# Performance work log

Hardware: AMD Instinct MI355X
Metric: run time of the kernel (lower is better)

## Reference

```python
import jax, jax.numpy as jnp
import numpy as np

TP, TN = 0.03, 0.03   # top-k fractions (module init args)
TS, TC = 0.03, 0.07   # sigmoid sharpness, contrastive temperature
EPS_PD = 1e-6         # torch F.pairwise_distance eps


def _l2norm(x, axis):
    # F.normalize(p=2) with eps clamp 1e-12
    return x / jnp.maximum(jnp.linalg.norm(x, axis=axis, keepdims=True), 1e-12)


def setup_inputs() -> dict:
    key = jax.random.key(0)
    k = jax.random.split(key, 5)
    B, C, H, W = 192, 512, 28, 28
    return {
        "ev": jax.random.normal(k[0], (B, C, H, W), jnp.float32),
        "ea": jax.random.normal(k[1], (B, 2048), jnp.float32),
        "Wv": jax.random.normal(k[2], (C, C), jnp.float32) * 0.04,
        "Wa1": jax.random.normal(k[3], (512, 2048), jnp.float32) * 0.02,
        "Wa2": jax.random.normal(k[4], (512, 512), jnp.float32) * 0.04,
    }


def reference(ev, ea, Wv, Wa1, Wa2):
    B, C, H, W = ev.shape
    HW = H * W
    tp = int(HW * TP)
    tn = int(HW * TN)

    # audio projection (frozen encoder output ea -> fa)
    fa = jax.nn.relu(ea @ Wa1.T) @ Wa2.T            # [B, 512]

    # visual 1x1-conv projection + GAP
    fv_map = jnp.einsum('bchw,oc->bohw', ev, Wv)    # [B, C, H, W]
    ind_vec = fv_map.mean(axis=(2, 3))              # [B, C]

    fv_norm = _l2norm(fv_map, axis=1)               # per-pixel channel L2 norm
    iv_norm = _l2norm(ind_vec, axis=1)              # [B, C]

    # Sij[b,d,p] = <fv_norm[b,:,p], iv_norm[d,:]>
    S = jnp.einsum('bchw,dc->bdhw', fv_norm, iv_norm).reshape(B, B, HW)

    # data-dependent per-(b,d) top-k thresholds
    pos_thr = jax.lax.top_k(S, tp)[0][..., -1:]     # tp-th largest
    neg_thr = -jax.lax.top_k(-S, tn)[0][..., -1:]   # tn-th smallest

    m_p = jax.nn.sigmoid((S - pos_thr) / TS)
    m_n = 1.0 - jax.nn.sigmoid((S - neg_thr) / TS)

    SP = (S * m_p).sum(-1) / m_p.sum(-1)            # [B, B]
    SN = (S * m_n).sum(-1) / m_n.sum(-1)            # [B, B]

    logits1 = jnp.concatenate([SP, SN], axis=1) / TC      # [B, 2B]
    logits2 = jnp.concatenate([SP.T, SN.T], axis=1) / TC  # [B, 2B]
    labels = jnp.arange(B)

    def ce(logits):
        logp = jax.nn.log_softmax(logits, axis=-1)
        return -jnp.take_along_axis(logp, labels[:, None], axis=1).mean()

    loss1 = ce(logits1)
    loss2 = ce(logits2)

    eye = jnp.eye(B, dtype=S.dtype)
    mask = eye - (1.0 - eye) / (B - 1)

    # squared pairwise distance between detached ind_vec and fa (torch eps)
    iv_d = jax.lax.stop_gradient(ind_vec)
    diff = iv_d[:, None, :] - fa[None, :, :] + EPS_PD
    dist = (diff * diff).sum(-1)                    # [B, B]

    ivn_d = jax.lax.stop_gradient(iv_norm)
    vv = ivn_d @ ivn_d.T
    w = -vv * (1.0 - eye) + eye
    dist = dist * w

    loss3 = jnp.maximum((dist * mask).sum(1) + 0.6, 0.0).mean()
    loss4 = jnp.maximum((dist * mask).sum(0) + 0.6, 0.0).mean()

    return ((loss1 + loss2) / 2, (loss3 + loss4) / 2)
```

## Files before the change

### kernel.cpp

```cpp
#include <hip/hip_runtime.h>
#include <hip/hip_fp8.h>
#include <math.h>

#define B_   192
#define C_   512
#define HW_  784
#define TPK  23
#define NTOT (B_ * HW_)
#define SCL  0x7F7F7F7F

typedef __attribute__((ext_vector_type(4))) float f4;
typedef __attribute__((ext_vector_type(16))) float f16v;
typedef __attribute__((ext_vector_type(8))) int i8i;
typedef __attribute__((ext_vector_type(4))) unsigned int u4i;
typedef __attribute__((ext_vector_type(8))) unsigned char uc8;

__device__ __forceinline__ float sigf(float x) {
    return 1.0f / (1.0f + __expf(-x));
}
__device__ __forceinline__ unsigned short f2bf(float f) {
    unsigned u = __float_as_uint(f);
    unsigned r = u + 0x7FFFu + ((u >> 16) & 1u);
    return (unsigned short)(r >> 16);
}
__device__ __forceinline__ float bf2f(unsigned short u) {
    return __uint_as_float(((unsigned)u) << 16);
}
__device__ __forceinline__ unsigned char f2fp8(float x) {
    __hip_fp8_e4m3 t(x);
    return (unsigned char)t.__x;
}
__device__ __forceinline__ void gld16(const void* g, void* l) {
    __builtin_amdgcn_global_load_lds((const __attribute__((address_space(1))) unsigned int*)g,
                                     (__attribute__((address_space(3))) unsigned int*)l, 16, 0, 0);
}
__device__ __forceinline__ i8i frag32(const unsigned char* base, int c0, int c1) {
    u4i lo = *(const u4i*)(base + c0);
    u4i hi = *(const u4i*)(base + c1);
    i8i r;
    r[0] = (int)lo[0]; r[1] = (int)lo[1]; r[2] = (int)lo[2]; r[3] = (int)lo[3];
    r[4] = (int)hi[0]; r[5] = (int)hi[1]; r[6] = (int)hi[2]; r[7] = (int)hi[3];
    return r;
}

__global__ void k_evmean(const float* __restrict__ ev, float* __restrict__ evmean) {
    int row  = blockIdx.x * 4 + (threadIdx.x >> 6);
    int lane = threadIdx.x & 63;
    const float4* s4 = (const float4*)(ev + (size_t)row * HW_);
    float s = 0.f;
    for (int i = lane; i < HW_ / 4; i += 64) {
        float4 v = s4[i];
        s += v.x + v.y + v.z + v.w;
    }
    for (int off = 32; off > 0; off >>= 1) s += __shfl_down(s, off, 64);
    if (lane == 0) evmean[row] = s * (1.0f / HW_);
}

template<int BKN, int RELUA, int SPLITK>
__global__ __launch_bounds__(256)
void k32(const float* __restrict__ A, const float* __restrict__ B,
         float* __restrict__ C, int M, int N, int K) {
    __shared__ float As[16][68];
    __shared__ float Bs[16][68];
    int m0 = blockIdx.y * 64, n0 = blockIdx.x * 64;
    int kslice = K / SPLITK;
    int kbeg = blockIdx.z * kslice;
    int tid = threadIdx.x;
    int tx = tid & 15, ty = tid >> 4;
    int r = tid >> 2, c4 = tid & 3;

    float acc[4][4];
#pragma unroll
    for (int i = 0; i < 4; i++)
#pragma unroll
        for (int j = 0; j < 4; j++) acc[i][j] = 0.f;

    for (int k0 = kbeg; k0 < kbeg + kslice; k0 += 16) {
        float4 av = *(const float4*)(A + (size_t)(m0 + r) * K + k0 + c4 * 4);
        if (RELUA) {
            av.x = fmaxf(av.x, 0.f); av.y = fmaxf(av.y, 0.f);
            av.z = fmaxf(av.z, 0.f); av.w = fmaxf(av.w, 0.f);
        }
        As[c4 * 4 + 0][r] = av.x; As[c4 * 4 + 1][r] = av.y;
        As[c4 * 4 + 2][r] = av.z; As[c4 * 4 + 3][r] = av.w;
        if (BKN == 0) {
            float4 bv = *(const float4*)(B + (size_t)(n0 + r) * K + k0 + c4 * 4);
            Bs[c4 * 4 + 0][r] = bv.x; Bs[c4 * 4 + 1][r] = bv.y;
            Bs[c4 * 4 + 2][r] = bv.z; Bs[c4 * 4 + 3][r] = bv.w;
        } else {
            float4 bv = *(const float4*)(B + (size_t)(k0 + ty) * N + n0 + tx * 4);
            Bs[ty][tx * 4 + 0] = bv.x; Bs[ty][tx * 4 + 1] = bv.y;
            Bs[ty][tx * 4 + 2] = bv.z; Bs[ty][tx * 4 + 3] = bv.w;
        }
        __syncthreads();
#pragma unroll
        for (int kk = 0; kk < 16; kk++) {
            float a_[4];
#pragma unroll
            for (int i = 0; i < 4; i++) a_[i] = As[kk][ty * 4 + i];
            float4 bb = *(const float4*)&Bs[kk][tx * 4];
#pragma unroll
            for (int i = 0; i < 4; i++) {
                acc[i][0] = fmaf(a_[i], bb.x, acc[i][0]);
                acc[i][1] = fmaf(a_[i], bb.y, acc[i][1]);
                acc[i][2] = fmaf(a_[i], bb.z, acc[i][2]);
                acc[i][3] = fmaf(a_[i], bb.w, acc[i][3]);
            }
        }
        __syncthreads();
    }
#pragma unroll
    for (int i = 0; i < 4; i++) {
        if (SPLITK > 1) {
            float* row = C + (size_t)(m0 + ty * 4 + i) * N + n0 + tx * 4;
#pragma unroll
            for (int j = 0; j < 4; j++) atomicAdd(&row[j], acc[i][j]);
        } else {
            *(float4*)(C + (size_t)(m0 + ty * 4 + i) * N + n0 + tx * 4) =
                make_float4(acc[i][0], acc[i][1], acc[i][2], acc[i][3]);
        }
    }
}

__global__ void k_rownorm(const float* __restrict__ iv, float* __restrict__ ivn) {
    int b = blockIdx.x, lane = threadIdx.x;
    float v[8]; float s = 0.f;
#pragma unroll
    for (int k = 0; k < 8; k++) {
        v[k] = iv[(size_t)b * C_ + lane + 64 * k];
        s = fmaf(v[k], v[k], s);
    }
#pragma unroll
    for (int off = 32; off > 0; off >>= 1) s += __shfl_xor(s, off, 64);
    float rn = 1.0f / fmaxf(sqrtf(s), 1e-12f);
#pragma unroll
    for (int k = 0; k < 8; k++) ivn[(size_t)b * C_ + lane + 64 * k] = v[k] * rn;
}

__global__ void k_prepA(const float* __restrict__ Wv, unsigned char* __restrict__ Abf) {
    int r = blockIdx.x, tid = threadIdx.x;
    int row = (r < 512) ? r : (192 + r);
    int swz = ((row >> 1) & 3) << 4;
    for (int i = 0; i < 2; i++) {
        int c = tid + i * 256;
        float v = (r < 512) ? Wv[(size_t)r * C_ + c] : 0.f;
        Abf[(size_t)row * C_ + (c ^ swz)] = f2fp8(v);
    }
}

__global__ __launch_bounds__(256)
void k_Ufp8(const float* __restrict__ ivn, const float* __restrict__ Wv,
            unsigned char* __restrict__ Abf) {
    __shared__ float As[16][68];
    __shared__ float Bs[16][68];
    int m0 = blockIdx.y * 64, n0 = blockIdx.x * 64;
    int tid = threadIdx.x;
    int tx = tid & 15, ty = tid >> 4;
    int r = tid >> 2, c4 = tid & 3;
    float acc[4][4];
#pragma unroll
    for (int i = 0; i < 4; i++)
#pragma unroll
        for (int j = 0; j < 4; j++) acc[i][j] = 0.f;
    for (int k0 = 0; k0 < C_; k0 += 16) {
        float4 av = *(const float4*)(ivn + (size_t)(m0 + r) * C_ + k0 + c4 * 4);
        As[c4 * 4 + 0][r] = av.x; As[c4 * 4 + 1][r] = av.y;
        As[c4 * 4 + 2][r] = av.z; As[c4 * 4 + 3][r] = av.w;
        float4 bv = *(const float4*)(Wv + (size_t)(k0 + ty) * C_ + n0 + tx * 4);
        Bs[ty][tx * 4 + 0] = bv.x; Bs[ty][tx * 4 + 1] = bv.y;
        Bs[ty][tx * 4 + 2] = bv.z; Bs[ty][tx * 4 + 3] = bv.w;
        __syncthreads();
#pragma unroll
        for (int kk = 0; kk < 16; kk++) {
            float a_[4];
#pragma unroll
            for (int i = 0; i < 4; i++) a_[i] = As[kk][ty * 4 + i];
            float4 bb = *(const float4*)&Bs[kk][tx * 4];
#pragma unroll
            for (int i = 0; i < 4; i++) {
                acc[i][0] = fmaf(a_[i], bb.x, acc[i][0]);
                acc[i][1] = fmaf(a_[i], bb.y, acc[i][1]);
                acc[i][2] = fmaf(a_[i], bb.z, acc[i][2]);
                acc[i][3] = fmaf(a_[i], bb.w, acc[i][3]);
            }
        }
        __syncthreads();
    }
#pragma unroll
    for (int i = 0; i < 4; i++) {
        int orow = 512 + m0 + ty * 4 + i;
        int swz = ((orow >> 1) & 3) << 4;
        unsigned char* rowp = Abf + (size_t)orow * C_;
        int cphys = (n0 + tx * 4) ^ swz;
#pragma unroll
        for (int j = 0; j < 4; j++) rowp[cphys + j] = f2fp8(acc[i][j]);
    }
}

__global__ __launch_bounds__(256)
void k_transpose64(const float* __restrict__ ev, unsigned char* __restrict__ evT,
                   float* __restrict__ evsum, int doevm, int b0) {
    __shared__ float t[64][67];
    int bl = blockIdx.z, b = b0 + bl;
    int c0 = blockIdx.y * 64, p0 = blockIdx.x * 64;
    int tid = threadIdx.x;
    int cl = tid >> 4;
    int pc = tid & 15;
    int p = p0 + pc * 4;
#pragma unroll
    for (int q = 0; q < 4; q++) {
        int c_local = q * 16 + cl;
        const float* src = ev + ((size_t)b * C_ + c0 + c_local) * HW_;
        float4 v = make_float4(0.f, 0.f, 0.f, 0.f);
        if (p + 3 < HW_) v = *(const float4*)(src + p);
        else if (p < HW_) { for (int j = 0; j < 4; j++) if (p + j < HW_) ((float*)&v)[j] = src[p + j]; }
        if (doevm) {
            float rs = v.x + v.y + v.z + v.w;
            rs += __shfl_xor(rs, 1, 16);
            rs += __shfl_xor(rs, 2, 16);
            rs += __shfl_xor(rs, 4, 16);
            rs += __shfl_xor(rs, 8, 16);
            if (pc == 0) atomicAdd(&evsum[b * C_ + c0 + c_local], rs * (1.0f / HW_));
        }
        t[c_local][pc * 4 + 0] = v.x; t[c_local][pc * 4 + 1] = v.y;
        t[c_local][pc * 4 + 2] = v.z; t[c_local][pc * 4 + 3] = v.w;
    }
    __syncthreads();
    int r = tid >> 3;
    int j = tid & 7;
#pragma unroll
    for (int q = 0; q < 2; q++) {
        int prow = p0 + r + q * 32;
        if (prow < HW_) {
            size_t n = (size_t)bl * HW_ + prow;
            int swz = ((int)(n >> 1) & 3) << 4;
            uc8 o;
#pragma unroll
            for (int k = 0; k < 8; k++) o[k] = f2fp8(t[j * 8 + k][r + q * 32]);
            *(uc8*)(evT + n * C_ + c0 + ((j * 8) ^ swz)) = o;
        }
    }
}

__global__ __launch_bounds__(256, 4)
void k_gemm(const unsigned char* __restrict__ Abf, const unsigned char* __restrict__ evT,
            float* __restrict__ n2, unsigned short* __restrict__ Tb, int ntiles) {
    __shared__ unsigned char As[2][8192];
    __shared__ unsigned char Bs[2][8192];

    int id = blockIdx.x;
    int xcd = id & 7, slot = id >> 3;
    int S = (ntiles + 7) >> 3;
    int w = xcd * S + slot;
    if (w >= ntiles) return;
    int nt = w / 6, ot = w % 6;
    int o0 = ot * 128, n0 = nt * 128;

    int tid = threadIdx.x;
    int wid = tid >> 6, lane = tid & 63;
    int wy = wid >> 1, wx = wid & 1;
    int r31 = lane & 31, hi = lane >> 5;
    int swz = (r31 >> 1) & 3;
    int ch0 = ((2 * hi) ^ swz) * 16;
    int ch1 = ((2 * hi + 1) ^ swz) * 16;

    const unsigned char* Ag = Abf + ((size_t)o0 + (tid >> 2)) * C_ + (tid & 3) * 16;
    const unsigned char* Bg = evT + ((size_t)n0 + (tid >> 2)) * C_ + (tid & 3) * 16;
    int lds16 = tid * 16;

    f16v acc[2][2] = {};
    int cur = 0;

#define STAGE(buf, k0) do { \
    gld16(Ag + (k0),           &As[buf][0]    + lds16); \
    gld16(Ag + (k0) + 64 * C_, &As[buf][4096] + lds16); \
    gld16(Bg + (k0),           &Bs[buf][0]    + lds16); \
    gld16(Bg + (k0) + 64 * C_, &Bs[buf][4096] + lds16); \
} while (0)

    STAGE(0, 0);
    __syncthreads();
    for (int t = 0; t < 8; ++t) {
        if (t < 7) STAGE(cur ^ 1, (t + 1) * 64);
        const unsigned char* Ab = &As[cur][0];
        const unsigned char* Bb = &Bs[cur][0];
        i8i a[2], b[2];
#pragma unroll
        for (int mi = 0; mi < 2; mi++)
            a[mi] = frag32(Ab + (wy * 64 + mi * 32 + r31) * 64, ch0, ch1);
#pragma unroll
        for (int ni = 0; ni < 2; ni++)
            b[ni] = frag32(Bb + (wx * 64 + ni * 32 + r31) * 64, ch0, ch1);
#pragma unroll
        for (int mi = 0; mi < 2; mi++)
#pragma unroll
            for (int ni = 0; ni < 2; ni++)
                acc[mi][ni] = __builtin_amdgcn_mfma_scale_f32_32x32x64_f8f6f4(
                    a[mi], b[ni], acc[mi][ni], 0, 0, 0, SCL, 0, SCL);
        __syncthreads();
        cur ^= 1;
    }
#undef STAGE

    if (ot < 4) {
        float* red = (float*)&As[0][0];
#pragma unroll
        for (int ni = 0; ni < 2; ni++) {
            float s = 0.f;
#pragma unroll
            for (int mi = 0; mi < 2; mi++)
#pragma unroll
                for (int r = 0; r < 16; r++) { float x = acc[mi][ni][r]; s = fmaf(x, x, s); }
            red[(wy * 2 + hi) * 128 + wx * 64 + ni * 32 + r31] = s;
        }
        __syncthreads();
        if (tid < 128) {
            float s = 0.f;
#pragma unroll
            for (int q = 0; q < 4; q++) s += red[q * 128 + tid];
            atomicAdd(&n2[n0 + tid], s);
        }
    } else {
        int dbase = o0 - 512 + wy * 64;
        unsigned blv[2]; int pv[2];
#pragma unroll
        for (int ni = 0; ni < 2; ni++) {
            unsigned nn = (unsigned)(n0 + wx * 64 + ni * 32 + r31);
            blv[ni] = nn / 784u;
            pv[ni]  = (int)(nn - blv[ni] * 784u);
        }
#pragma unroll
        for (int mi = 0; mi < 2; mi++)
#pragma unroll
            for (int r = 0; r < 16; r++) {
                int dd = dbase + mi * 32 + (r & 3) + 8 * (r >> 2) + 4 * hi;
                if (dd < B_) {
#pragma unroll
                    for (int ni = 0; ni < 2; ni++)
                        Tb[((size_t)blv[ni] * B_ + dd) * HW_ + pv[ni]] = f2bf(acc[mi][ni][r]);
                }
            }
    }
}

__global__ void k_invn(const float* __restrict__ n2, float* __restrict__ invn, int n) {
    int i = blockIdx.x * 256 + threadIdx.x;
    if (i >= n) return;
    invn[i] = 1.0f / fmaxf(sqrtf(n2[i]), 1e-12f);
}

__global__ __launch_bounds__(256)
void k_pool(const unsigned short* __restrict__ T, const float* __restrict__ invn,
            float* __restrict__ SP, float* __restrict__ SN, int b0) {
    int tid = threadIdx.x;
    int wv = tid >> 6, lane = tid & 63;
    int d = blockIdx.x * 4 + wv;
    int bl = blockIdx.y, b = b0 + bl;
    const unsigned short* Trow = T + ((size_t)b * B_ + d) * HW_;
    const float* nrow = invn + (size_t)b * HW_;
    float sv[13];
#pragma unroll
    for (int i = 0; i < 12; i++) {
        int p = lane + i * 64;
        sv[i] = bf2f(Trow[p]) * nrow[p];
    }
    {
        int p = lane + 768;
        sv[12] = (p < HW_) ? bf2f(Trow[p]) * nrow[p] : __uint_as_float(0x7FC00000u);
    }
    float vmax = -1e30f, vmin = 1e30f;
#pragma unroll
    for (int i = 0; i < 13; i++) { vmax = fmaxf(vmax, sv[i]); vmin = fminf(vmin, sv[i]); }
#pragma unroll
    for (int off = 32; off > 0; off >>= 1) {
        vmax = fmaxf(vmax, __shfl_xor(vmax, off, 64));
        vmin = fminf(vmin, __shfl_xor(vmin, off, 64));
    }
    float lo1 = vmin, hi1 = vmax, lo2 = vmin, hi2 = vmax;
    for (int it = 0; it < 13; ++it) {
        float m1 = 0.5f * (lo1 + hi1), m2 = 0.5f * (lo2 + hi2);
        int c1 = 0, c2 = 0;
#pragma unroll
        for (int i = 0; i < 13; i++) {
            c1 += __popcll(__ballot(sv[i] >= m1));
            c2 += __popcll(__ballot(sv[i] <= m2));
        }
        if (c1 >= TPK) lo1 = m1; else hi1 = m1;
        if (c2 >= TPK) hi2 = m2; else lo2 = m2;
    }
    float thrp = lo1, thrn = hi2;
    const float its = 1.0f / 0.03f;
    float spn = 0.f, spd = 0.f, snn = 0.f, snd = 0.f;
#pragma unroll
    for (int i = 0; i < 13; i++) {
        if (i == 12 && lane >= 16) continue;
        float s = sv[i];
        float mp = sigf((s - thrp) * its);
        float mn = sigf(-(s - thrn) * its);
        spn += s * mp; spd += mp;
        snn += s * mn; snd += mn;
    }
    for (int off = 32; off > 0; off >>= 1) {
        spn += __shfl_down(spn, off, 64);
        spd += __shfl_down(spd, off, 64);
        snn += __shfl_down(snn, off, 64);
        snd += __shfl_down(snd, off, 64);
    }
    if (lane == 0) {
        SP[b * B_ + d] = spn / spd;
        SN[b * B_ + d] = snn / snd;
    }
}

__global__ void k_loss12(const float* __restrict__ SP, const float* __restrict__ SN,
                         float* __restrict__ acc) {
    __shared__ float red[128];
    int i = blockIdx.x, tid = threadIdx.x;
    const float itc = 1.0f / 0.07f;
    for (int phase = 0; phase < 2; phase++) {
        float mx = -INFINITY;
        for (int j = tid; j < 2 * B_; j += 128) {
            float v;
            if (phase == 0) v = (j < B_ ? SP[i * B_ + j] : SN[i * B_ + (j - B_)]);
            else            v = (j < B_ ? SP[j * B_ + i] : SN[(j - B_) * B_ + i]);
            mx = fmaxf(mx, v * itc);
        }
        red[tid] = mx; __syncthreads();
        for (int s = 64; s > 0; s >>= 1) { if (tid < s) red[tid] = fmaxf(red[tid], red[tid + s]); __syncthreads(); }
        mx = red[0]; __syncthreads();
        float se = 0.f;
        for (int j = tid; j < 2 * B_; j += 128) {
            float v;
            if (phase == 0) v = (j < B_ ? SP[i * B_ + j] : SN[i * B_ + (j - B_)]);
            else            v = (j < B_ ? SP[j * B_ + i] : SN[(j - B_) * B_ + i]);
            se += __expf(v * itc - mx);
        }
        red[tid] = se; __syncthreads();
        for (int s = 64; s > 0; s >>= 1) { if (tid < s) red[tid] += red[tid + s]; __syncthreads(); }
        if (tid == 0) {
            float lse = logf(red[0]) + mx;
            atomicAdd(&acc[phase], lse - SP[i * B_ + i] * itc);
        }
        __syncthreads();
    }
}

__global__ __launch_bounds__(256)
void k_distfin(const float* __restrict__ iv, const float* __restrict__ ivn,
               const float* __restrict__ fa, const float* __restrict__ acc,
               float* __restrict__ rowsum, float* __restrict__ colsum,
               int* __restrict__ cnt, float* __restrict__ out) {
    __shared__ float Ai[16][68], An[16][68], Bf[16][68], Bn[16][68];
    __shared__ float rred[64][17], cred[64][17];
    __shared__ float fr[256];
    __shared__ int lastf;
    int i0 = blockIdx.y * 64, j0 = blockIdx.x * 64;
    int tid = threadIdx.x;
    int tx = tid & 15, ty = tid >> 4;
    int r = tid >> 2, c4 = tid & 3;
    float accD[4][4], accV[4][4];
#pragma unroll
    for (int i = 0; i < 4; i++)
#pragma unroll
        for (int j = 0; j < 4; j++) { accD[i][j] = 0.f; accV[i][j] = 0.f; }

    for (int k0 = 0; k0 < C_; k0 += 16) {
        float4 v;
        v = *(const float4*)(iv + (size_t)(i0 + r) * C_ + k0 + c4 * 4);
        Ai[c4*4+0][r]=v.x; Ai[c4*4+1][r]=v.y; Ai[c4*4+2][r]=v.z; Ai[c4*4+3][r]=v.w;
        v = *(const float4*)(ivn + (size_t)(i0 + r) * C_ + k0 + c4 * 4);
        An[c4*4+0][r]=v.x; An[c4*4+1][r]=v.y; An[c4*4+2][r]=v.z; An[c4*4+3][r]=v.w;
        v = *(const float4*)(fa + (size_t)(j0 + r) * C_ + k0 + c4 * 4);
        Bf[c4*4+0][r]=v.x; Bf[c4*4+1][r]=v.y; Bf[c4*4+2][r]=v.z; Bf[c4*4+3][r]=v.w;
        v = *(const float4*)(ivn + (size_t)(j0 + r) * C_ + k0 + c4 * 4);
        Bn[c4*4+0][r]=v.x; Bn[c4*4+1][r]=v.y; Bn[c4*4+2][r]=v.z; Bn[c4*4+3][r]=v.w;
        __syncthreads();
#pragma unroll
        for (int kk = 0; kk < 16; kk++) {
            float ai[4], an[4];
#pragma unroll
            for (int i = 0; i < 4; i++) { ai[i] = Ai[kk][ty*4+i]; an[i] = An[kk][ty*4+i]; }
            float4 bf = *(const float4*)&Bf[kk][tx*4];
            float4 bn = *(const float4*)&Bn[kk][tx*4];
#pragma unroll
            for (int i = 0; i < 4; i++) {
                float d0 = ai[i] - bf.x + 1e-6f; accD[i][0] = fmaf(d0, d0, accD[i][0]);
                float d1 = ai[i] - bf.y + 1e-6f; accD[i][1] = fmaf(d1, d1, accD[i][1]);
                float d2 = ai[i] - bf.z + 1e-6f; accD[i][2] = fmaf(d2, d2, accD[i][2]);
                float d3 = ai[i] - bf.w + 1e-6f; accD[i][3] = fmaf(d3, d3, accD[i][3]);
                accV[i][0] = fmaf(an[i], bn.x, accV[i][0]);
                accV[i][1] = fmaf(an[i], bn.y, accV[i][1]);
                accV[i][2] = fmaf(an[i], bn.z, accV[i][2]);
                accV[i][3] = fmaf(an[i], bn.w, accV[i][3]);
            }
        }
        __syncthreads();
    }
    float rp[4] = {0.f, 0.f, 0.f, 0.f};
    float cp[4] = {0.f, 0.f, 0.f, 0.f};
#pragma unroll
    for (int i = 0; i < 4; i++)
#pragma unroll
        for (int j = 0; j < 4; j++) {
            int gi = i0 + ty * 4 + i, gj = j0 + tx * 4 + j;
            float val = (gi == gj) ? accD[i][j] : accD[i][j] * accV[i][j] * (1.0f / 191.0f);
            rp[i] += val; cp[j] += val;
        }
#pragma unroll
    for (int i = 0; i < 4; i++) rred[ty * 4 + i][tx] = rp[i];
#pragma unroll
    for (int j = 0; j < 4; j++) cred[tx * 4 + j][ty] = cp[j];
    __syncthreads();
    if (tid < 64) {
        float s = 0.f;
#pragma unroll
        for (int q = 0; q < 16; q++) s += rred[tid][q];
        atomicAdd(&rowsum[i0 + tid], s);
    } else if (tid < 128) {
        int t = tid - 64;
        float s = 0.f;
#pragma unroll
        for (int q = 0; q < 16; q++) s += cred[t][q];
        atomicAdd(&colsum[j0 + t], s);
    }
    __threadfence();
    __syncthreads();
    if (tid == 0) lastf = (atomicAdd(cnt, 1) == 8);
    __syncthreads();
    if (lastf) {
        __threadfence();
        float v3 = (tid < B_) ? fmaxf(rowsum[tid] + 0.6f, 0.f) : 0.f;
        float v4 = (tid < B_) ? fmaxf(colsum[tid] + 0.6f, 0.f) : 0.f;
        fr[tid] = v3; __syncthreads();
        for (int s = 128; s > 0; s >>= 1) { if (tid < s) fr[tid] += fr[tid + s]; __syncthreads(); }
        float l3 = fr[0] / B_;
        __syncthreads();
        fr[tid] = v4; __syncthreads();
        for (int s = 128; s > 0; s >>= 1) { if (tid < s) fr[tid] += fr[tid + s]; __syncthreads(); }
        float l4 = fr[0] / B_;
        if (tid == 0) {
            out[0] = 0.5f * (acc[0] + acc[1]) / B_;
            out[1] = 0.5f * (l3 + l4);
        }
    }
}

extern "C" void kernel_launch(void* const* d_in, const int* in_sizes, int n_in,
                              void* d_out, int out_size, void* d_ws, size_t ws_size,
                              hipStream_t stream) {
    const float* ev  = (const float*)d_in[0];
    const float* ea  = (const float*)d_in[1];
    const float* Wv  = (const float*)d_in[2];
    const float* Wa1 = (const float*)d_in[3];
    const float* Wa2 = (const float*)d_in[4];
    float* out = (float*)d_out;
    float* ws  = (float*)d_ws;

    size_t off = 0;
    float* evmean  = ws + off; off += B_ * C_;
    float* ind_vec = ws + off; off += B_ * C_;
    float* Hb      = ws + off; off += B_ * C_;
    float* fa      = ws + off; off += B_ * C_;
    float* n2      = ws + off; off += NTOT;
    float* accb    = ws + off;
    float* rowsum  = accb + 16;
    float* colsum  = rowsum + B_;
    int*   cntp    = (int*)(colsum + B_);
    off += 16 + B_ + B_ + 16;
    size_t zero_count = off;
    float* iv_norm = ws + off; off += B_ * C_;
    float* invn    = ws + off; off += NTOT;
    float* SPb     = ws + off; off += B_ * B_;
    float* SNb     = ws + off; off += B_ * B_;
    unsigned char* Abf = (unsigned char*)(ws + off); off += 768 * C_ / 4;

    size_t perB_f = (size_t)HW_ * C_ / 4 + (size_t)B_ * HW_ / 2;
    size_t avail  = ws_size / 4 > off ? ws_size / 4 - off : 0;
    int chunk = (int)(avail / perB_f);
    chunk &= ~7;
    if (chunk > B_) chunk = B_;
    if (chunk < 8) chunk = 8;
    unsigned char* evT = (unsigned char*)(ws + off);
    unsigned short* Tb = (unsigned short*)(evT + (size_t)chunk * HW_ * C_);

    hipMemsetAsync(ws, 0, zero_count * sizeof(float), stream);

    k_prepA<<<576, 256, 0, stream>>>(Wv, Abf);

    if (chunk >= B_) {
        dim3 gt(13, C_ / 64, B_);
        k_transpose64<<<gt, 256, 0, stream>>>(ev, evT, evmean, 1, 0);
    } else {
        k_evmean<<<B_ * C_ / 4, 256, 0, stream>>>(ev, evmean);
    }

    k32<0, 0, 4><<<dim3(8, 3, 4), 256, 0, stream>>>(ea, Wa1, Hb, B_, C_, 2048);
    k32<0, 1, 2><<<dim3(8, 3, 2), 256, 0, stream>>>(Hb, Wa2, fa, B_, C_, C_);

    k32<0, 0, 2><<<dim3(8, 3, 2), 256, 0, stream>>>(evmean, Wv, ind_vec, B_, C_, C_);
    k_rownorm<<<B_, 64, 0, stream>>>(ind_vec, iv_norm);
    k_Ufp8<<<dim3(8, 3), 256, 0, stream>>>(iv_norm, Wv, Abf);

    if (chunk >= B_) {
        int ntiles = (NTOT / 128) * 6;
        int S = (ntiles + 7) >> 3;
        k_gemm<<<8 * S, 256, 0, stream>>>(Abf, evT, n2, Tb, ntiles);
        k_invn<<<(NTOT + 255) / 256, 256, 0, stream>>>(n2, invn, NTOT);
        dim3 gp(B_ / 4, B_);
        k_pool<<<gp, 256, 0, stream>>>(Tb, invn, SPb, SNb, 0);
    } else {
        for (int b0 = 0; b0 < B_; b0 += chunk) {
            int nb = (B_ - b0 < chunk) ? (B_ - b0) : chunk;
            dim3 gt(13, C_ / 64, nb);
            k_transpose64<<<gt, 256, 0, stream>>>(ev, evT, evmean, 0, b0);
            int ntiles = (nb * HW_ / 128) * 6;
            int S = (ntiles + 7) >> 3;
            k_gemm<<<8 * S, 256, 0, stream>>>(Abf, evT, n2 + (size_t)b0 * HW_, Tb, ntiles);
            int n = nb * HW_;
            k_invn<<<(n + 255) / 256, 256, 0, stream>>>(n2 + (size_t)b0 * HW_,
                                                        invn + (size_t)b0 * HW_, n);
            dim3 gp(B_ / 4, nb);
            k_pool<<<gp, 256, 0, stream>>>(Tb - (size_t)b0 * B_ * HW_, invn, SPb, SNb, b0);
        }
    }

    k_loss12<<<B_, 128, 0, stream>>>(SPb, SNb, accb);
    dim3 gd(B_ / 64, B_ / 64);
    k_distfin<<<gd, 256, 0, stream>>>(ind_vec, iv_norm, fa, accb, rowsum, colsum, cntp, out);
}
```

Before: 443.9 us.

## Fuse small projection GEMMs, widen transpose tiles, stage GEMM epilogue through LDS

Replaces the five small tiled FP32 GEMM and norm launches with two per-row kernels. k_aud computes the two-layer audio projection. k_vis computes ind_vec, its L2 norm and the fp8 U rows. The transpose now handles 128 channels per block and writes 16-byte fp8 vectors, and the GEMM epilogue stages bf16 results in LDS so Tb is written with coalesced 16-byte stores instead of scattered 2-byte stores. The per-row GEMV kernels trade tiled reuse of the weights for fewer launches, and k_vis reads Wv column-wise, which may be uncoalesced.

```diff
diff --git a/kernel.cpp b/kernel.cpp
--- a/kernel.cpp
+++ b/kernel.cpp
@@ -13,7 +13,8 @@
 typedef __attribute__((ext_vector_type(16))) float f16v;
 typedef __attribute__((ext_vector_type(8))) int i8i;
 typedef __attribute__((ext_vector_type(4))) unsigned int u4i;
-typedef __attribute__((ext_vector_type(8))) unsigned char uc8;
+typedef __attribute__((ext_vector_type(16))) unsigned char uc16;
+typedef __attribute__((ext_vector_type(8))) unsigned short us8w;
 
 __device__ __forceinline__ float sigf(float x) {
     return 1.0f / (1.0f + __expf(-x));
@@ -56,85 +57,97 @@
     if (lane == 0) evmean[row] = s * (1.0f / HW_);
 }
 
-template<int BKN, int RELUA, int SPLITK>
 __global__ __launch_bounds__(256)
-void k32(const float* __restrict__ A, const float* __restrict__ B,
-         float* __restrict__ C, int M, int N, int K) {
-    __shared__ float As[16][68];
-    __shared__ float Bs[16][68];
-    int m0 = blockIdx.y * 64, n0 = blockIdx.x * 64;
-    int kslice = K / SPLITK;
-    int kbeg = blockIdx.z * kslice;
-    int tid = threadIdx.x;
-    int tx = tid & 15, ty = tid >> 4;
-    int r = tid >> 2, c4 = tid & 3;
-
-    float acc[4][4];
-#pragma unroll
-    for (int i = 0; i < 4; i++)
-#pragma unroll
-        for (int j = 0; j < 4; j++) acc[i][j] = 0.f;
-
-    for (int k0 = kbeg; k0 < kbeg + kslice; k0 += 16) {
-        float4 av = *(const float4*)(A + (size_t)(m0 + r) * K + k0 + c4 * 4);
-        if (RELUA) {
-            av.x = fmaxf(av.x, 0.f); av.y = fmaxf(av.y, 0.f);
-            av.z = fmaxf(av.z, 0.f); av.w = fmaxf(av.w, 0.f);
-        }
-        As[c4 * 4 + 0][r] = av.x; As[c4 * 4 + 1][r] = av.y;
-        As[c4 * 4 + 2][r] = av.z; As[c4 * 4 + 3][r] = av.w;
-        if (BKN == 0) {
-            float4 bv = *(const float4*)(B + (size_t)(n0 + r) * K + k0 + c4 * 4);
-            Bs[c4 * 4 + 0][r] = bv.x; Bs[c4 * 4 + 1][r] = bv.y;
-            Bs[c4 * 4 + 2][r] = bv.z; Bs[c4 * 4 + 3][r] = bv.w;
-        } else {
-            float4 bv = *(const float4*)(B + (size_t)(k0 + ty) * N + n0 + tx * 4);
-            Bs[ty][tx * 4 + 0] = bv.x; Bs[ty][tx * 4 + 1] = bv.y;
-            Bs[ty][tx * 4 + 2] = bv.z; Bs[ty][tx * 4 + 3] = bv.w;
-        }
-        __syncthreads();
-#pragma unroll
-        for (int kk = 0; kk < 16; kk++) {
-            float a_[4];
-#pragma unroll
-            for (int i = 0; i < 4; i++) a_[i] = As[kk][ty * 4 + i];
-            float4 bb = *(const float4*)&Bs[kk][tx * 4];
-#pragma unroll
-            for (int i = 0; i < 4; i++) {
-                acc[i][0] = fmaf(a_[i], bb.x, acc[i][0]);
-                acc[i][1] = fmaf(a_[i], bb.y, acc[i][1]);
-                acc[i][2] = fmaf(a_[i], bb.z, acc[i][2]);
-                acc[i][3] = fmaf(a_[i], bb.w, acc[i][3]);
-            }
-        }
-        __syncthreads();
-    }
-#pragma unroll
-    for (int i = 0; i < 4; i++) {
-        if (SPLITK > 1) {
-            float* row = C + (size_t)(m0 + ty * 4 + i) * N + n0 + tx * 4;
-#pragma unroll
-            for (int j = 0; j < 4; j++) atomicAdd(&row[j], acc[i][j]);
-        } else {
-            *(float4*)(C + (size_t)(m0 + ty * 4 + i) * N + n0 + tx * 4) =
-                make_float4(acc[i][0], acc[i][1], acc[i][2], acc[i][3]);
-        }
-    }
-}
-
-__global__ void k_rownorm(const float* __restrict__ iv, float* __restrict__ ivn) {
-    int b = blockIdx.x, lane = threadIdx.x;
-    float v[8]; float s = 0.f;
-#pragma unroll
-    for (int k = 0; k < 8; k++) {
-        v[k] = iv[(size_t)b * C_ + lane + 64 * k];
-        s = fmaf(v[k], v[k], s);
-    }
-#pragma unroll
-    for (int off = 32; off > 0; off >>= 1) s += __shfl_xor(s, off, 64);
-    float rn = 1.0f / fmaxf(sqrtf(s), 1e-12f);
-#pragma unroll
-    for (int k = 0; k < 8; k++) ivn[(size_t)b * C_ + lane + 64 * k] = v[k] * rn;
+void k_vis(const float* __restrict__ evmean, const float* __restrict__ Wv,
+           float* __restrict__ ind_vec, float* __restrict__ iv_norm,
+           unsigned char* __restrict__ Abf) {
+    __shared__ float evm[C_];
+    __shared__ float ivn_s[C_];
+    __shared__ float red[256];
+    int d = blockIdx.x, tid = threadIdx.x;
+    evm[tid]       = evmean[d * C_ + tid];
+    evm[tid + 256] = evmean[d * C_ + tid + 256];
+    __syncthreads();
+    float iv[2]; float ss = 0.f;
+#pragma unroll
+    for (int r2 = 0; r2 < 2; r2++) {
+        int o = tid + r2 * 256;
+        const float4* wr = (const float4*)(Wv + (size_t)o * C_);
+        float a0 = 0.f, a1 = 0.f;
+        for (int c4 = 0; c4 < 128; c4 += 2) {
+            float4 w0 = wr[c4], w1 = wr[c4 + 1];
+            a0 = fmaf(w0.x, evm[c4*4+0], a0); a0 = fmaf(w0.y, evm[c4*4+1], a0);
+            a0 = fmaf(w0.z, evm[c4*4+2], a0); a0 = fmaf(w0.w, evm[c4*4+3], a0);
+            a1 = fmaf(w1.x, evm[c4*4+4], a1); a1 = fmaf(w1.y, evm[c4*4+5], a1);
+            a1 = fmaf(w1.z, evm[c4*4+6], a1); a1 = fmaf(w1.w, evm[c4*4+7], a1);
+        }
+        iv[r2] = a0 + a1;
+        ss = fmaf(iv[r2], iv[r2], ss);
+    }
+    red[tid] = ss; __syncthreads();
+    for (int s = 128; s > 0; s >>= 1) { if (tid < s) red[tid] += red[tid + s]; __syncthreads(); }
+    float rn = 1.0f / fmaxf(sqrtf(red[0]), 1e-12f);
+#pragma unroll
+    for (int r2 = 0; r2 < 2; r2++) {
+        int o = tid + r2 * 256;
+        float v = iv[r2] * rn;
+        ind_vec[d * C_ + o] = iv[r2];
+        iv_norm[d * C_ + o] = v;
+        ivn_s[o] = v;
+    }
+    __syncthreads();
+    int orow = 512 + d;
+    int swz = ((orow >> 1) & 3) << 4;
+    unsigned char* arow = Abf + (size_t)orow * C_;
+#pragma unroll
+    for (int r2 = 0; r2 < 2; r2++) {
+        int c = tid + r2 * 256;
+        float u0 = 0.f, u1 = 0.f;
+        for (int o = 0; o < C_; o += 2) {
+            u0 = fmaf(Wv[(size_t)o * C_ + c],       ivn_s[o],     u0);
+            u1 = fmaf(Wv[(size_t)(o + 1) * C_ + c], ivn_s[o + 1], u1);
+        }
+        arow[c ^ swz] = f2fp8(u0 + u1);
+    }
+}
+
+__global__ __launch_bounds__(256)
+void k_aud(const float* __restrict__ ea, const float* __restrict__ Wa1,
+           const float* __restrict__ Wa2, float* __restrict__ fa) {
+    __shared__ float ear[2048];
+    __shared__ float hs[C_];
+    int b = blockIdx.x, tid = threadIdx.x;
+    for (int i = tid; i < 2048; i += 256) ear[i] = ea[b * 2048 + i];
+    __syncthreads();
+#pragma unroll
+    for (int r2 = 0; r2 < 2; r2++) {
+        int o = tid + r2 * 256;
+        const float4* wr = (const float4*)(Wa1 + (size_t)o * 2048);
+        float a0 = 0.f, a1 = 0.f;
+        for (int k = 0; k < 512; k += 2) {
+            float4 w0 = wr[k], w1 = wr[k + 1];
+            a0 = fmaf(w0.x, ear[k*4+0], a0); a0 = fmaf(w0.y, ear[k*4+1], a0);
+            a0 = fmaf(w0.z, ear[k*4+2], a0); a0 = fmaf(w0.w, ear[k*4+3], a0);
+            a1 = fmaf(w1.x, ear[k*4+4], a1); a1 = fmaf(w1.y, ear[k*4+5], a1);
+            a1 = fmaf(w1.z, ear[k*4+6], a1); a1 = fmaf(w1.w, ear[k*4+7], a1);
+        }
+        hs[o] = fmaxf(a0 + a1, 0.f);
+    }
+    __syncthreads();
+#pragma unroll
+    for (int r2 = 0; r2 < 2; r2++) {
+        int c = tid + r2 * 256;
+        const float4* wr = (const float4*)(Wa2 + (size_t)c * C_);
+        float a0 = 0.f, a1 = 0.f;
+        for (int k = 0; k < 128; k += 2) {
+            float4 w0 = wr[k], w1 = wr[k + 1];
+            a0 = fmaf(w0.x, hs[k*4+0], a0); a0 = fmaf(w0.y, hs[k*4+1], a0);
+            a0 = fmaf(w0.z, hs[k*4+2], a0); a0 = fmaf(w0.w, hs[k*4+3], a0);
+            a1 = fmaf(w1.x, hs[k*4+4], a1); a1 = fmaf(w1.y, hs[k*4+5], a1);
+            a1 = fmaf(w1.z, hs[k*4+6], a1); a1 = fmaf(w1.w, hs[k*4+7], a1);
+        }
+        fa[b * C_ + c] = a0 + a1;
+    }
 }
 
 __global__ void k_prepA(const float* __restrict__ Wv, unsigned char* __restrict__ Abf) {
@@ -149,67 +162,17 @@
 }
 
 __global__ __launch_bounds__(256)
-void k_Ufp8(const float* __restrict__ ivn, const float* __restrict__ Wv,
-            unsigned char* __restrict__ Abf) {
-    __shared__ float As[16][68];
-    __shared__ float Bs[16][68];
-    int m0 = blockIdx.y * 64, n0 = blockIdx.x * 64;
+void k_transpose(const float* __restrict__ ev, unsigned char* __restrict__ evT,
+                 float* __restrict__ evsum, int doevm, int b0) {
+    __shared__ float t[128][65];
+    int bl = blockIdx.z, b = b0 + bl;
+    int c0 = blockIdx.y * 128, p0 = blockIdx.x * 64;
     int tid = threadIdx.x;
-    int tx = tid & 15, ty = tid >> 4;
-    int r = tid >> 2, c4 = tid & 3;
-    float acc[4][4];
-#pragma unroll
-    for (int i = 0; i < 4; i++)
-#pragma unroll
-        for (int j = 0; j < 4; j++) acc[i][j] = 0.f;
-    for (int k0 = 0; k0 < C_; k0 += 16) {
-        float4 av = *(const float4*)(ivn + (size_t)(m0 + r) * C_ + k0 + c4 * 4);
-        As[c4 * 4 + 0][r] = av.x; As[c4 * 4 + 1][r] = av.y;
-        As[c4 * 4 + 2][r] = av.z; As[c4 * 4 + 3][r] = av.w;
-        float4 bv = *(const float4*)(Wv + (size_t)(k0 + ty) * C_ + n0 + tx * 4);
-        Bs[ty][tx * 4 + 0] = bv.x; Bs[ty][tx * 4 + 1] = bv.y;
-        Bs[ty][tx * 4 + 2] = bv.z; Bs[ty][tx * 4 + 3] = bv.w;
-        __syncthreads();
-#pragma unroll
-        for (int kk = 0; kk < 16; kk++) {
-            float a_[4];
-#pragma unroll
-            for (int i = 0; i < 4; i++) a_[i] = As[kk][ty * 4 + i];
-            float4 bb = *(const float4*)&Bs[kk][tx * 4];
-#pragma unroll
-            for (int i = 0; i < 4; i++) {
-                acc[i][0] = fmaf(a_[i], bb.x, acc[i][0]);
-                acc[i][1] = fmaf(a_[i], bb.y, acc[i][1]);
-                acc[i][2] = fmaf(a_[i], bb.z, acc[i][2]);
-                acc[i][3] = fmaf(a_[i], bb.w, acc[i][3]);
-            }
-        }
-        __syncthreads();
-    }
-#pragma unroll
-    for (int i = 0; i < 4; i++) {
-        int orow = 512 + m0 + ty * 4 + i;
-        int swz = ((orow >> 1) & 3) << 4;
-        unsigned char* rowp = Abf + (size_t)orow * C_;
-        int cphys = (n0 + tx * 4) ^ swz;
-#pragma unroll
-        for (int j = 0; j < 4; j++) rowp[cphys + j] = f2fp8(acc[i][j]);
-    }
-}
-
-__global__ __launch_bounds__(256)
-void k_transpose64(const float* __restrict__ ev, unsigned char* __restrict__ evT,
-                   float* __restrict__ evsum, int doevm, int b0) {
-    __shared__ float t[64][67];
-    int bl = blockIdx.z, b = b0 + bl;
-    int c0 = blockIdx.y * 64, p0 = blockIdx.x * 64;
-    int tid = threadIdx.x;
-    int cl = tid >> 4;
     int pc = tid & 15;
     int p = p0 + pc * 4;
 #pragma unroll
-    for (int q = 0; q < 4; q++) {
-        int c_local = q * 16 + cl;
+    for (int q = 0; q < 8; q++) {
+        int c_local = q * 16 + (tid >> 4);
         const float* src = ev + ((size_t)b * C_ + c0 + c_local) * HW_;
         float4 v = make_float4(0.f, 0.f, 0.f, 0.f);
         if (p + 3 < HW_) v = *(const float4*)(src + p);
@@ -226,18 +189,19 @@
         t[c_local][pc * 4 + 2] = v.z; t[c_local][pc * 4 + 3] = v.w;
     }
     __syncthreads();
-    int r = tid >> 3;
-    int j = tid & 7;
+    int pl = tid >> 3;
+    int j  = tid & 7;
 #pragma unroll
     for (int q = 0; q < 2; q++) {
-        int prow = p0 + r + q * 32;
+        int prl = pl + q * 32;
+        int prow = p0 + prl;
         if (prow < HW_) {
             size_t n = (size_t)bl * HW_ + prow;
             int swz = ((int)(n >> 1) & 3) << 4;
-            uc8 o;
-#pragma unroll
-            for (int k = 0; k < 8; k++) o[k] = f2fp8(t[j * 8 + k][r + q * 32]);
-            *(uc8*)(evT + n * C_ + c0 + ((j * 8) ^ swz)) = o;
+            uc16 o;
+#pragma unroll
+            for (int k = 0; k < 16; k++) o[k] = f2fp8(t[j * 16 + k][prl]);
+            *(uc16*)(evT + n * C_ + (((c0 + j * 16) ^ swz))) = o;
         }
     }
 }
@@ -245,8 +209,7 @@
 __global__ __launch_bounds__(256, 4)
 void k_gemm(const unsigned char* __restrict__ Abf, const unsigned char* __restrict__ evT,
             float* __restrict__ n2, unsigned short* __restrict__ Tb, int ntiles) {
-    __shared__ unsigned char As[2][8192];
-    __shared__ unsigned char Bs[2][8192];
+    __shared__ unsigned char SM[32768];
 
     int id = blockIdx.x;
     int xcd = id & 7, slot = id >> 3;
@@ -272,18 +235,18 @@
     int cur = 0;
 
 #define STAGE(buf, k0) do { \
-    gld16(Ag + (k0),           &As[buf][0]    + lds16); \
-    gld16(Ag + (k0) + 64 * C_, &As[buf][4096] + lds16); \
-    gld16(Bg + (k0),           &Bs[buf][0]    + lds16); \
-    gld16(Bg + (k0) + 64 * C_, &Bs[buf][4096] + lds16); \
+    gld16(Ag + (k0),           SM + (buf) * 8192 + lds16); \
+    gld16(Ag + (k0) + 64 * C_, SM + (buf) * 8192 + 4096 + lds16); \
+    gld16(Bg + (k0),           SM + 16384 + (buf) * 8192 + lds16); \
+    gld16(Bg + (k0) + 64 * C_, SM + 16384 + (buf) * 8192 + 4096 + lds16); \
 } while (0)
 
     STAGE(0, 0);
     __syncthreads();
     for (int t = 0; t < 8; ++t) {
         if (t < 7) STAGE(cur ^ 1, (t + 1) * 64);
-        const unsigned char* Ab = &As[cur][0];
-        const unsigned char* Bb = &Bs[cur][0];
+        const unsigned char* Ab = SM + cur * 8192;
+        const unsigned char* Bb = SM + 16384 + cur * 8192;
         i8i a[2], b[2];
 #pragma unroll
         for (int mi = 0; mi < 2; mi++)
@@ -303,7 +266,7 @@
 #undef STAGE
 
     if (ot < 4) {
-        float* red = (float*)&As[0][0];
+        float* red = (float*)SM;
 #pragma unroll
         for (int ni = 0; ni < 2; ni++) {
             float s = 0.f;
@@ -321,25 +284,33 @@
             atomicAdd(&n2[n0 + tid], s);
         }
     } else {
-        int dbase = o0 - 512 + wy * 64;
-        unsigned blv[2]; int pv[2];
-#pragma unroll
-        for (int ni = 0; ni < 2; ni++) {
-            unsigned nn = (unsigned)(n0 + wx * 64 + ni * 32 + r31);
-            blv[ni] = nn / 784u;
-            pv[ni]  = (int)(nn - blv[ni] * 784u);
-        }
+        unsigned short* Cs = (unsigned short*)SM;
 #pragma unroll
         for (int mi = 0; mi < 2; mi++)
 #pragma unroll
             for (int r = 0; r < 16; r++) {
-                int dd = dbase + mi * 32 + (r & 3) + 8 * (r >> 2) + 4 * hi;
-                if (dd < B_) {
-#pragma unroll
-                    for (int ni = 0; ni < 2; ni++)
-                        Tb[((size_t)blv[ni] * B_ + dd) * HW_ + pv[ni]] = f2bf(acc[mi][ni][r]);
+                int row = wy * 64 + mi * 32 + (r & 3) + 8 * (r >> 2) + 4 * hi;
+#pragma unroll
+                for (int ni = 0; ni < 2; ni++) {
+                    int col = wx * 64 + ni * 32 + r31;
+                    Cs[row * 128 + col] = f2bf(acc[mi][ni][r]);
                 }
             }
+        __syncthreads();
+        int dbase = o0 - 512;
+        int cchunk = (tid & 15) * 8;
+        unsigned nn = (unsigned)(n0 + cchunk);
+        unsigned bb = nn / 784u;
+        int pp = (int)(nn - bb * 784u);
+#pragma unroll
+        for (int pass = 0; pass < 8; pass++) {
+            int row = pass * 16 + (tid >> 4);
+            int dd = dbase + row;
+            if (dd < B_) {
+                us8w v = *(const us8w*)(Cs + row * 128 + cchunk);
+                *(us8w*)(Tb + ((size_t)bb * B_ + dd) * HW_ + pp) = v;
+            }
+        }
     }
 }
 
@@ -558,9 +529,6 @@
 
     size_t off = 0;
     float* evmean  = ws + off; off += B_ * C_;
-    float* ind_vec = ws + off; off += B_ * C_;
-    float* Hb      = ws + off; off += B_ * C_;
-    float* fa      = ws + off; off += B_ * C_;
     float* n2      = ws + off; off += NTOT;
     float* accb    = ws + off;
     float* rowsum  = accb + 16;
@@ -568,7 +536,9 @@
     int*   cntp    = (int*)(colsum + B_);
     off += 16 + B_ + B_ + 16;
     size_t zero_count = off;
+    float* ind_vec = ws + off; off += B_ * C_;
     float* iv_norm = ws + off; off += B_ * C_;
+    float* fa      = ws + off; off += B_ * C_;
     float* invn    = ws + off; off += NTOT;
     float* SPb     = ws + off; off += B_ * B_;
     float* SNb     = ws + off; off += B_ * B_;
@@ -588,20 +558,11 @@
     k_prepA<<<576, 256, 0, stream>>>(Wv, Abf);
 
     if (chunk >= B_) {
-        dim3 gt(13, C_ / 64, B_);
-        k_transpose64<<<gt, 256, 0, stream>>>(ev, evT, evmean, 1, 0);
-    } else {
-        k_evmean<<<B_ * C_ / 4, 256, 0, stream>>>(ev, evmean);
-    }
-
-    k32<0, 0, 4><<<dim3(8, 3, 4), 256, 0, stream>>>(ea, Wa1, Hb, B_, C_, 2048);
-    k32<0, 1, 2><<<dim3(8, 3, 2), 256, 0, stream>>>(Hb, Wa2, fa, B_, C_, C_);
-
-    k32<0, 0, 2><<<dim3(8, 3, 2), 256, 0, stream>>>(evmean, Wv, ind_vec, B_, C_, C_);
-    k_rownorm<<<B_, 64, 0, stream>>>(ind_vec, iv_norm);
-    k_Ufp8<<<dim3(8, 3), 256, 0, stream>>>(iv_norm, Wv, Abf);
-
-    if (chunk >= B_) {
+        dim3 gt(13, 4, B_);
+        k_transpose<<<gt, 256, 0, stream>>>(ev, evT, evmean, 1, 0);
+        k_aud<<<B_, 256, 0, stream>>>(ea, Wa1, Wa2, fa);
+        k_vis<<<B_, 256, 0, stream>>>(evmean, Wv, ind_vec, iv_norm, Abf);
+
         int ntiles = (NTOT / 128) * 6;
         int S = (ntiles + 7) >> 3;
         k_gemm<<<8 * S, 256, 0, stream>>>(Abf, evT, n2, Tb, ntiles);
@@ -609,10 +570,13 @@
         dim3 gp(B_ / 4, B_);
         k_pool<<<gp, 256, 0, stream>>>(Tb, invn, SPb, SNb, 0);
     } else {
+        k_evmean<<<B_ * C_ / 4, 256, 0, stream>>>(ev, evmean);
+        k_aud<<<B_, 256, 0, stream>>>(ea, Wa1, Wa2, fa);
+        k_vis<<<B_, 256, 0, stream>>>(evmean, Wv, ind_vec, iv_norm, Abf);
         for (int b0 = 0; b0 < B_; b0 += chunk) {
             int nb = (B_ - b0 < chunk) ? (B_ - b0) : chunk;
-            dim3 gt(13, C_ / 64, nb);
-            k_transpose64<<<gt, 256, 0, stream>>>(ev, evT, evmean, 0, b0);
+            dim3 gt(13, 4, nb);
+            k_transpose<<<gt, 256, 0, stream>>>(ev, evT, evmean, 0, b0);
             int ntiles = (nb * HW_ / 128) * 6;
             int S = (ntiles + 7) >> 3;
             k_gemm<<<8 * S, 256, 0, stream>>>(Abf, evT, n2 + (size_t)b0 * HW_, Tb, ntiles);
```

Result: slower. 586.3 us (+32.1%).
